# Kernel optimization log

Hardware: AMD Instinct MI355X
Metric: run time of the kernel (lower is better)

The kernel has to match this reference:

```python
import jax, jax.numpy as jnp
import numpy as np

KS = 5          # B-spline kernel_size per pseudo-coordinate dim
DIM = 2         # pseudo-coordinate dimensionality
NUM_GRAPHS = 64


def spline_conv(x, src, dst, edge_attr, W, root, bias):
    """Degree-1 open B-spline conv (torch-spline-conv semantics, aggr='mean').
    x: [N,Cin], edge_attr: [E,DIM] in [0,1], W: [KS**DIM,Cin,Cout]."""
    N = x.shape[0]
    E = src.shape[0]
    v = edge_attr * (KS - 1)                                   # [E,DIM]
    k_lo = jnp.clip(jnp.floor(v), 0, KS - 2).astype(jnp.int32) # lower knot index
    frac = v - k_lo.astype(v.dtype)                            # [E,DIM]
    # Precompute x @ W_k for all K kernel weights per node: [N,K,Cout]
    xW = jnp.einsum('nc,kco->nko', x, W)
    msg = jnp.zeros((E, W.shape[2]), x.dtype)
    # 2^DIM = 4 nonzero basis products for degree-1 splines
    for bits in ((0, 0), (0, 1), (1, 0), (1, 1)):
        b = jnp.ones((E,), x.dtype)
        wi = jnp.zeros((E,), jnp.int32)
        stride = 1
        for d, bit in enumerate(bits):
            b = b * (frac[:, d] if bit else (1.0 - frac[:, d]))
            wi = wi + (k_lo[:, d] + bit) * stride
            stride *= KS
        msg = msg + b[:, None] * xW[src, wi]                   # gather [E,Cout]
    agg = jax.ops.segment_sum(msg, dst, num_segments=N)
    deg = jax.ops.segment_sum(jnp.ones((E,), x.dtype), dst, num_segments=N)
    agg = agg / jnp.maximum(deg, 1.0)[:, None]                 # mean aggregation
    return agg + x @ root + bias


def setup_inputs() -> dict:
    key = jax.random.key(0)
    ks = jax.random.split(key, 12)
    N, E = 20000, 320000
    Cin, H, O = 1, 32, 10
    K = KS * KS
    p = lambda k, s: jax.random.normal(k, s, jnp.float32) * 0.1
    return {
        'x': jax.random.normal(ks[0], (N, Cin), jnp.float32),
        'edge_attr': jax.random.uniform(ks[1], (E, DIM), jnp.float32),
        'W1': p(ks[2], (K, Cin, H)), 'root1': p(ks[3], (Cin, H)), 'b1': jnp.zeros((H,), jnp.float32),
        'W2': p(ks[4], (K, H, 2 * H)), 'root2': p(ks[5], (H, 2 * H)), 'b2': jnp.zeros((2 * H,), jnp.float32),
        'Wf1': p(ks[6], (2 * H, 128)), 'bf1': jnp.zeros((128,), jnp.float32),
        'Wf2': p(ks[7], (128, O)), 'bf2': jnp.zeros((O,), jnp.float32),
        'edge_index': jax.random.randint(ks[8], (2, E), 0, N),
        'batch': jnp.sort(jax.random.randint(ks[9], (N,), 0, NUM_GRAPHS)),
    }


def reference(x, edge_attr, W1, root1, b1, W2, root2, b2, Wf1, bf1, Wf2, bf2, edge_index, batch):
    src, dst = edge_index[0], edge_index[1]
    h = jax.nn.relu(spline_conv(x, src, dst, edge_attr, W1, root1, b1))
    h = jax.nn.relu(spline_conv(h, src, dst, edge_attr, W2, root2, b2))
    # global mean pool over graphs
    gsum = jax.ops.segment_sum(h, batch, num_segments=NUM_GRAPHS)
    cnt = jax.ops.segment_sum(jnp.ones((h.shape[0],), h.dtype), batch, num_segments=NUM_GRAPHS)
    g = gsum / jnp.maximum(cnt, 1.0)[:, None]
    g = jax.nn.relu(g @ Wf1 + bf1)
    return jax.nn.log_softmax(g @ Wf2 + bf2, axis=1)
```

## Files before the change

### kernel.cpp

```cpp
#include <hip/hip_runtime.h>
#include <hip/hip_fp16.h>
#include <math.h>

#define KK 25
#define H1C 32
#define H2C 64
#define FCC 128
#define NCLS 10
#define NG 64
#define M1 32
#define M2 16

typedef _Float16 v8h __attribute__((ext_vector_type(8)));
typedef _Float16 v4h __attribute__((ext_vector_type(4)));
typedef float v4f __attribute__((ext_vector_type(4)));

__global__ __launch_bounds__(256) void deg_kernel(
    const int* __restrict__ edge_index, int E,
    int* __restrict__ degi,
    const float* __restrict__ W2, __half* __restrict__ W2t) {
    int i = blockIdx.x * 256 + threadIdx.x;
    if (i < KK * H2C * H1C) {
        int c = i & 31, o = (i >> 5) & 63, k = i >> 11;
        W2t[i] = __float2half(W2[(k * H1C + c) * H2C + o]);
    }
    if (i < E) atomicAdd(&degi[edge_index[E + i]], 1);
}

__global__ void scan1_kernel(const int* __restrict__ degi, int N,
                             int* __restrict__ incl, int* __restrict__ bsum) {
    __shared__ int s[256];
    int tid = threadIdx.x;
    int i = blockIdx.x * 256 + tid;
    int v = (i < N) ? degi[i] : 0;
    s[tid] = v;
    __syncthreads();
    for (int off = 1; off < 256; off <<= 1) {
        int t = (tid >= off) ? s[tid - off] : 0;
        __syncthreads();
        s[tid] += t;
        __syncthreads();
    }
    if (i < N) incl[i] = s[tid];
    if (tid == 255) bsum[blockIdx.x] = s[255];
}

__global__ void scan2_kernel(int* __restrict__ bsum, int nb) {
    __shared__ int s[256];
    int tid = threadIdx.x;
    int v = (tid < nb) ? bsum[tid] : 0;
    s[tid] = v;
    __syncthreads();
    for (int off = 1; off < 256; off <<= 1) {
        int t = (tid >= off) ? s[tid - off] : 0;
        __syncthreads();
        s[tid] += t;
        __syncthreads();
    }
    if (tid < nb) bsum[tid] = s[tid] - v;
}

__global__ void scan3_kernel(const int* __restrict__ incl, const int* __restrict__ degi,
                             const int* __restrict__ bsum, int N,
                             int* __restrict__ rowst, int* __restrict__ cur) {
    int i = blockIdx.x * 256 + threadIdx.x;
    if (i >= N) return;
    int r = incl[i] - degi[i] + bsum[blockIdx.x];
    rowst[i] = r;
    cur[i] = r;
}

__global__ void bucket_kernel(const float* __restrict__ edge_attr,
                              const int* __restrict__ edge_index, int E,
                              int* __restrict__ cur, int4* __restrict__ es) {
    int e = blockIdx.x * blockDim.x + threadIdx.x;
    if (e >= E) return;
    float v0 = edge_attr[2 * e + 0] * 4.0f;
    float v1 = edge_attr[2 * e + 1] * 4.0f;
    int k0 = (int)floorf(v0); k0 = min(max(k0, 0), 3);
    int k1 = (int)floorf(v1); k1 = min(max(k1, 0), 3);
    float f0 = v0 - (float)k0, f1 = v1 - (float)k1;
    int dst = edge_index[E + e];
    int pos = atomicAdd(&cur[dst], 1);
    es[pos] = make_int4(edge_index[e], (dst << 8) | (k0 + 5 * k1),
                        __float_as_int(f0), __float_as_int(f1));
}

__global__ __launch_bounds__(256) void l1_kernel(
    const float* __restrict__ x,
    const int* __restrict__ rowst, const int* __restrict__ degi,
    const int4* __restrict__ es,
    const float* __restrict__ W1, const float* __restrict__ root1,
    const float* __restrict__ b1, int N, int E,
    float* __restrict__ h1, __half* __restrict__ h1f) {
    __shared__ float w1s[KK * H1C];
    __shared__ float agg1[M1 * H1C];
    __shared__ int4 eb[8][32];
    __shared__ float xb[8][32];
    int tid = threadIdx.x;
    for (int i = tid; i < KK * H1C; i += 256) w1s[i] = W1[i];
    for (int i = tid; i < M1 * H1C; i += 256) agg1[i] = 0.0f;
    __syncthreads();
    int g = tid >> 5, o = tid & 31;
    int n0 = blockIdx.x * M1;
    int blkBeg = rowst[n0];
    int blkEnd = (n0 + M1 < N) ? rowst[n0 + M1] : E;
    int total = blkEnd - blkBeg;
    int per = (total + 7) >> 3;
    int wBeg = blkBeg + g * per;
    int wEnd = min(blkEnd, wBeg + per);
    int curDst = -1;
    float acc = 0.0f;
    for (int base = wBeg; base < wEnd; base += 32) {
        int m = min(32, wEnd - base);
        if (o < m) {
            int4 ed = es[base + o];
            eb[g][o] = ed;
            xb[g][o] = x[ed.x];
        }
        for (int j = 0; j < m; j++) {
            int4 ed = eb[g][j];
            float xs = xb[g][j];
            int dst = ed.y >> 8;
            if (dst != curDst) {
                if (curDst >= 0) atomicAdd(&agg1[(curDst - n0) * H1C + o], acc);
                acc = 0.0f;
                curDst = dst;
            }
            float f0 = __int_as_float(ed.z), f1 = __int_as_float(ed.w);
            float g0 = 1.0f - f0, g1 = 1.0f - f1;
            int kb = (ed.y & 0xff) << 5;
            float coef = g0 * g1 * w1s[kb + o] + f0 * g1 * w1s[kb + 32 + o] +
                         g0 * f1 * w1s[kb + 160 + o] + f0 * f1 * w1s[kb + 192 + o];
            acc = fmaf(xs, coef, acc);
        }
    }
    if (curDst >= 0) atomicAdd(&agg1[(curDst - n0) * H1C + o], acc);
    __syncthreads();
#pragma unroll
    for (int i = 0; i < 4; i++) {
        int ln = g + 8 * i;
        int n = n0 + ln;
        if (n < N) {
            float rdeg = 1.0f / fmaxf((float)degi[n], 1.0f);
            float hv = fmaxf(agg1[ln * H1C + o] * rdeg + x[n] * root1[o] + b1[o], 0.0f);
            h1[n * H1C + o] = hv;
            h1f[n * H1C + o] = __float2half(hv);
        }
    }
}

__global__ __launch_bounds__(256) void xw2m_kernel(
    const __half* __restrict__ h1f,
    const __half* __restrict__ W2t,
    int N, __half* __restrict__ xph) {
    int wv = threadIdx.x >> 6;
    int lane = threadIdx.x & 63;
    int r15 = lane & 15, quad = lane >> 4;
    int n0 = blockIdx.x * 16;
    int o0 = wv * 16;
    v8h bfrag = {};
    int bn = n0 + r15;
    bool wr = bn < N;
    if (wr) bfrag = *(const v8h*)(h1f + (size_t)bn * H1C + quad * 8);
    size_t baseoff = (size_t)bn * (KK * H2C) + o0 + (quad << 2);
    for (int k = 0; k < KK; k++) {
        v8h afrag = *(const v8h*)(W2t + ((k << 6) + o0 + r15) * H1C + quad * 8);
        v4f acc = {};
        acc = __builtin_amdgcn_mfma_f32_16x16x32_f16(afrag, bfrag, acc, 0, 0, 0);
        if (wr) {
            v4h hv;
            hv[0] = (_Float16)acc[0];
            hv[1] = (_Float16)acc[1];
            hv[2] = (_Float16)acc[2];
            hv[3] = (_Float16)acc[3];
            *(v4h*)(xph + baseoff + (k << 6)) = hv;
        }
    }
}

__global__ __launch_bounds__(256) void l2_kernel(
    const float* __restrict__ h1,
    const int* __restrict__ rowst, const int* __restrict__ degi,
    const int4* __restrict__ es,
    const unsigned* __restrict__ xphu,
    const float* __restrict__ root2, const float* __restrict__ b2,
    const int* __restrict__ batch,
    int N, int E, float* __restrict__ gsum) {
    __shared__ float agg[M2 * H2C];
    __shared__ int4 eb[4][64];
    int tid = threadIdx.x;
    for (int i = tid; i < M2 * H2C; i += 256) agg[i] = 0.0f;
    __syncthreads();
    int w = tid >> 6, lane = tid & 63;
    int o2 = lane & 31, eh = lane >> 5;
    int n0 = blockIdx.x * M2;
    int blkBeg = rowst[n0];
    int blkEnd = (n0 + M2 < N) ? rowst[n0 + M2] : E;
    int total = blkEnd - blkBeg;
    int per = (total + 3) >> 2;
    int wBeg = blkBeg + w * per;
    int wEnd = min(blkEnd, wBeg + per);
    int curDst = -1;
    float ax = 0.0f, ay = 0.0f;
    for (int base = wBeg; base < wEnd; base += 64) {
        int m = min(64, wEnd - base);
        if (lane < m) eb[w][lane] = es[base + lane];
        for (int j = 0; j < m; j += 2) {
            int jj = j + eh;
            bool act = jj < m;
            int4 ed = eb[w][act ? jj : j];
            const unsigned* p = xphu + (size_t)ed.x * (KK * H2C / 2) +
                                ((ed.y & 0xff) << 5) + o2;
            unsigned t0 = p[0], t1 = p[32], t2 = p[160], t3 = p[192];
            if (act) {
                int dst = ed.y >> 8;
                if (dst != curDst) {
                    if (curDst >= 0) {
                        atomicAdd(&agg[(curDst - n0) * H2C + 2 * o2], ax);
                        atomicAdd(&agg[(curDst - n0) * H2C + 2 * o2 + 1], ay);
                    }
                    ax = ay = 0.0f;
                    curDst = dst;
                }
                float f0 = __int_as_float(ed.z), f1 = __int_as_float(ed.w);
                float g0 = 1.0f - f0, g1 = 1.0f - f1;
                float b0 = g0 * g1, b1 = f0 * g1, bb2 = g0 * f1, b3 = f0 * f1;
                __half2 h0 = *(__half2*)&t0, h1v = *(__half2*)&t1;
                __half2 h2 = *(__half2*)&t2, h3 = *(__half2*)&t3;
                ax = fmaf(b0, __low2float(h0), ax);  ay = fmaf(b0, __high2float(h0), ay);
                ax = fmaf(b1, __low2float(h1v), ax); ay = fmaf(b1, __high2float(h1v), ay);
                ax = fmaf(bb2, __low2float(h2), ax); ay = fmaf(bb2, __high2float(h2), ay);
                ax = fmaf(b3, __low2float(h3), ax);  ay = fmaf(b3, __high2float(h3), ay);
            }
        }
    }
    if (curDst >= 0) {
        atomicAdd(&agg[(curDst - n0) * H2C + 2 * o2], ax);
        atomicAdd(&agg[(curDst - n0) * H2C + 2 * o2 + 1], ay);
    }
    __syncthreads();

#pragma unroll
    for (int i = 0; i < 4; i++) {
        int ln = w + 4 * i;
        int n = n0 + ln;
        if (n < N) {
            float rd = 1.0f / fmaxf((float)degi[n], 1.0f);
            float v = agg[ln * H2C + lane] * rd + b2[lane];
            const float* hr = h1 + n * H1C;
#pragma unroll 8
            for (int c = 0; c < H1C; c++) v = fmaf(hr[c], root2[c * H2C + lane], v);
            agg[ln * H2C + lane] = fmaxf(v, 0.0f);
        } else {
            agg[ln * H2C + lane] = 0.0f;
        }
    }
    __syncthreads();

    if (tid < H2C) {
        float run = 0.0f;
        int curg = batch[n0];
        for (int ln = 0; ln < M2; ln++) {
            int n = n0 + ln;
            if (n >= N) break;
            int gg = batch[n];
            if (gg != curg) {
                atomicAdd(&gsum[curg * H2C + tid], run);
                run = 0.0f;
                curg = gg;
            }
            run += agg[ln * H2C + tid];
        }
        atomicAdd(&gsum[curg * H2C + tid], run);
    }
}

__global__ void head_kernel(const float* __restrict__ gsum,
                            const int* __restrict__ batch, int N,
                            const float* __restrict__ Wf1, const float* __restrict__ bf1,
                            const float* __restrict__ Wf2, const float* __restrict__ bf2,
                            float* __restrict__ out) {
    __shared__ float gc[H2C];
    __shared__ float t1[FCC];
    __shared__ float lg[NCLS];
    __shared__ float lse;
    __shared__ float scnt;
    int g = blockIdx.x, tid = threadIdx.x;
    if (tid == 0) {
        int lo = 0, hi = N;
        while (lo < hi) { int m = (lo + hi) >> 1; if (batch[m] < g) lo = m + 1; else hi = m; }
        int lb = lo;
        lo = 0; hi = N;
        while (lo < hi) { int m = (lo + hi) >> 1; if (batch[m] <= g) lo = m + 1; else hi = m; }
        scnt = (float)(lo - lb);
    }
    __syncthreads();
    if (tid < H2C) gc[tid] = gsum[g * H2C + tid] / fmaxf(scnt, 1.0f);
    __syncthreads();
    {
        float acc = bf1[tid];
        for (int c = 0; c < H2C; c++) acc += gc[c] * Wf1[c * FCC + tid];
        t1[tid] = fmaxf(acc, 0.0f);
    }
    __syncthreads();
    if (tid < NCLS) {
        float acc = bf2[tid];
        for (int j = 0; j < FCC; j++) acc += t1[j] * Wf2[j * NCLS + tid];
        lg[tid] = acc;
    }
    __syncthreads();
    if (tid == 0) {
        float m = lg[0];
        for (int c = 1; c < NCLS; c++) m = fmaxf(m, lg[c]);
        float s = 0.0f;
        for (int c = 0; c < NCLS; c++) s += expf(lg[c] - m);
        lse = m + logf(s);
    }
    __syncthreads();
    if (tid < NCLS) out[g * NCLS + tid] = lg[tid] - lse;
}

extern "C" void kernel_launch(void* const* d_in, const int* in_sizes, int n_in,
                              void* d_out, int out_size, void* d_ws, size_t ws_size,
                              hipStream_t stream) {
    const float* x          = (const float*)d_in[0];
    const float* edge_attr  = (const float*)d_in[1];
    const float* W1         = (const float*)d_in[2];
    const float* root1      = (const float*)d_in[3];
    const float* b1         = (const float*)d_in[4];
    const float* W2         = (const float*)d_in[5];
    const float* root2      = (const float*)d_in[6];
    const float* b2         = (const float*)d_in[7];
    const float* Wf1        = (const float*)d_in[8];
    const float* bf1        = (const float*)d_in[9];
    const float* Wf2        = (const float*)d_in[10];
    const float* bf2        = (const float*)d_in[11];
    const int*   edge_index = (const int*)d_in[12];
    const int*   batch      = (const int*)d_in[13];
    float* out = (float*)d_out;

    const int N = in_sizes[13];
    const int E = in_sizes[12] / 2;
    const int NB = (N + 255) / 256;

    int4*     es   = (int4*)d_ws;
    unsigned* xphu = (unsigned*)(es + E);
    __half*   w2t  = (__half*)(xphu + (size_t)N * 800);
    __half*   h1f  = w2t + KK * H2C * H1C;
    float* gsum  = (float*)(h1f + (size_t)N * H1C);
    int*   degi  = (int*)(gsum + NG * H2C);
    int*   rowst = degi + N;
    int*   cur   = rowst + N;
    int*   incl  = cur + N;
    int*   bsum  = incl + N;
    float* h1    = (float*)(bsum + 256);

    hipMemsetAsync(gsum, 0, (size_t)NG * H2C * sizeof(float) + (size_t)N * sizeof(int),
                   stream);

    const int W2TN = KK * H2C * H1C;
    int degBlocks = (max(E, W2TN) + 255) / 256;
    deg_kernel<<<degBlocks, 256, 0, stream>>>(edge_index, E, degi, W2, w2t);

    scan1_kernel<<<NB, 256, 0, stream>>>(degi, N, incl, bsum);
    scan2_kernel<<<1, 256, 0, stream>>>(bsum, NB);
    scan3_kernel<<<NB, 256, 0, stream>>>(incl, degi, bsum, N, rowst, cur);

    bucket_kernel<<<(E + 255) / 256, 256, 0, stream>>>(edge_attr, edge_index, E, cur, es);

    l1_kernel<<<(N + M1 - 1) / M1, 256, 0, stream>>>(
        x, rowst, degi, es, W1, root1, b1, N, E, h1, h1f);

    xw2m_kernel<<<(N + 15) / 16, 256, 0, stream>>>(h1f, w2t, N, (__half*)xphu);

    l2_kernel<<<(N + M2 - 1) / M2, 256, 0, stream>>>(
        h1, rowst, degi, es, xphu, root2, b2, batch, N, E, gsum);

    head_kernel<<<NG, FCC, 0, stream>>>(gsum, batch, N, Wf1, bf1, Wf2, bf2, out);
}
```

Measured before the change: 215.4 us.

## Aggregate basis-weighted inputs before the W2 matmul and fuse the layer-2 kernels

Reorders layer 2 from transform-then-aggregate to aggregate-then-transform. Each block scatters basis-weighted h1 features into a per-node shared-memory buffer of size K*Cin using LDS atomics. It then applies W2 and root2 with MFMA inside the same kernel. This removes the large per-node xW intermediate (N*25*64 halfs) and its global write/read traffic, along with the fp32 h1 copy. In exchange it adds four LDS float atomics per edge-channel, uses about 51KB of shared memory per block, which may limit occupancy, and rounds the aggregated sums to fp16 before the MFMA.

Result: slower. 425.8 us (+97.6%).

```diff
diff --git a/kernel.cpp b/kernel.cpp
--- a/kernel.cpp
+++ b/kernel.cpp
@@ -10,19 +10,24 @@
 #define NG 64
 #define M1 32
 #define M2 16
+#define SROW 804
 
 typedef _Float16 v8h __attribute__((ext_vector_type(8)));
-typedef _Float16 v4h __attribute__((ext_vector_type(4)));
 typedef float v4f __attribute__((ext_vector_type(4)));
 
 __global__ __launch_bounds__(256) void deg_kernel(
     const int* __restrict__ edge_index, int E,
     int* __restrict__ degi,
-    const float* __restrict__ W2, __half* __restrict__ W2t) {
+    const float* __restrict__ W2, __half* __restrict__ W2o,
+    const float* __restrict__ root2, __half* __restrict__ r2t) {
     int i = blockIdx.x * 256 + threadIdx.x;
-    if (i < KK * H2C * H1C) {
-        int c = i & 31, o = (i >> 5) & 63, k = i >> 11;
-        W2t[i] = __float2half(W2[(k * H1C + c) * H2C + o]);
+    if (i < KK * H1C * H2C) {
+        int o = i & 63, kc = i >> 6;
+        W2o[(size_t)o * (KK * H1C) + kc] = __float2half(W2[i]);
+    }
+    if (i < H1C * H2C) {
+        int o = i & 63, c = i >> 6;
+        r2t[o * H1C + c] = __float2half(root2[i]);
     }
     if (i < E) atomicAdd(&degi[edge_index[E + i]], 1);
 }
@@ -92,7 +97,7 @@
     const int4* __restrict__ es,
     const float* __restrict__ W1, const float* __restrict__ root1,
     const float* __restrict__ b1, int N, int E,
-    float* __restrict__ h1, __half* __restrict__ h1f) {
+    __half* __restrict__ h1f) {
     __shared__ float w1s[KK * H1C];
     __shared__ float agg1[M1 * H1C];
     __shared__ int4 eb[8][32];
@@ -144,54 +149,27 @@
         if (n < N) {
             float rdeg = 1.0f / fmaxf((float)degi[n], 1.0f);
             float hv = fmaxf(agg1[ln * H1C + o] * rdeg + x[n] * root1[o] + b1[o], 0.0f);
-            h1[n * H1C + o] = hv;
             h1f[n * H1C + o] = __float2half(hv);
         }
     }
 }
 
-__global__ __launch_bounds__(256) void xw2m_kernel(
+__global__ __launch_bounds__(256) void l2f_kernel(
     const __half* __restrict__ h1f,
-    const __half* __restrict__ W2t,
-    int N, __half* __restrict__ xph) {
-    int wv = threadIdx.x >> 6;
-    int lane = threadIdx.x & 63;
-    int r15 = lane & 15, quad = lane >> 4;
-    int n0 = blockIdx.x * 16;
-    int o0 = wv * 16;
-    v8h bfrag = {};
-    int bn = n0 + r15;
-    bool wr = bn < N;
-    if (wr) bfrag = *(const v8h*)(h1f + (size_t)bn * H1C + quad * 8);
-    size_t baseoff = (size_t)bn * (KK * H2C) + o0 + (quad << 2);
-    for (int k = 0; k < KK; k++) {
-        v8h afrag = *(const v8h*)(W2t + ((k << 6) + o0 + r15) * H1C + quad * 8);
-        v4f acc = {};
-        acc = __builtin_amdgcn_mfma_f32_16x16x32_f16(afrag, bfrag, acc, 0, 0, 0);
-        if (wr) {
-            v4h hv;
-            hv[0] = (_Float16)acc[0];
-            hv[1] = (_Float16)acc[1];
-            hv[2] = (_Float16)acc[2];
-            hv[3] = (_Float16)acc[3];
-            *(v4h*)(xph + baseoff + (k << 6)) = hv;
-        }
-    }
-}
-
-__global__ __launch_bounds__(256) void l2_kernel(
-    const float* __restrict__ h1,
     const int* __restrict__ rowst, const int* __restrict__ degi,
     const int4* __restrict__ es,
-    const unsigned* __restrict__ xphu,
-    const float* __restrict__ root2, const float* __restrict__ b2,
+    const __half* __restrict__ W2o,
+    const __half* __restrict__ r2t,
+    const float* __restrict__ b2,
     const int* __restrict__ batch,
     int N, int E, float* __restrict__ gsum) {
-    __shared__ float agg[M2 * H2C];
+    __shared__ float S[M2 * SROW];
     __shared__ int4 eb[4][64];
+    __shared__ float h2s[M2 * H2C];
     int tid = threadIdx.x;
-    for (int i = tid; i < M2 * H2C; i += 256) agg[i] = 0.0f;
-    __syncthreads();
+    for (int i = tid; i < M2 * SROW; i += 256) S[i] = 0.0f;
+    __syncthreads();
+
     int w = tid >> 6, lane = tid & 63;
     int o2 = lane & 31, eh = lane >> 5;
     int n0 = blockIdx.x * M2;
@@ -201,60 +179,66 @@
     int per = (total + 3) >> 2;
     int wBeg = blkBeg + w * per;
     int wEnd = min(blkEnd, wBeg + per);
-    int curDst = -1;
-    float ax = 0.0f, ay = 0.0f;
+
     for (int base = wBeg; base < wEnd; base += 64) {
         int m = min(64, wEnd - base);
         if (lane < m) eb[w][lane] = es[base + lane];
         for (int j = 0; j < m; j += 2) {
             int jj = j + eh;
-            bool act = jj < m;
-            int4 ed = eb[w][act ? jj : j];
-            const unsigned* p = xphu + (size_t)ed.x * (KK * H2C / 2) +
-                                ((ed.y & 0xff) << 5) + o2;
-            unsigned t0 = p[0], t1 = p[32], t2 = p[160], t3 = p[192];
-            if (act) {
-                int dst = ed.y >> 8;
-                if (dst != curDst) {
-                    if (curDst >= 0) {
-                        atomicAdd(&agg[(curDst - n0) * H2C + 2 * o2], ax);
-                        atomicAdd(&agg[(curDst - n0) * H2C + 2 * o2 + 1], ay);
-                    }
-                    ax = ay = 0.0f;
-                    curDst = dst;
-                }
+            if (jj < m) {
+                int4 ed = eb[w][jj];
+                float xv = __half2float(h1f[(size_t)ed.x * H1C + o2]);
+                int dstl = (ed.y >> 8) - n0;
+                int kb = ed.y & 0xff;
                 float f0 = __int_as_float(ed.z), f1 = __int_as_float(ed.w);
                 float g0 = 1.0f - f0, g1 = 1.0f - f1;
-                float b0 = g0 * g1, b1 = f0 * g1, bb2 = g0 * f1, b3 = f0 * f1;
-                __half2 h0 = *(__half2*)&t0, h1v = *(__half2*)&t1;
-                __half2 h2 = *(__half2*)&t2, h3 = *(__half2*)&t3;
-                ax = fmaf(b0, __low2float(h0), ax);  ay = fmaf(b0, __high2float(h0), ay);
-                ax = fmaf(b1, __low2float(h1v), ax); ay = fmaf(b1, __high2float(h1v), ay);
-                ax = fmaf(bb2, __low2float(h2), ax); ay = fmaf(bb2, __high2float(h2), ay);
-                ax = fmaf(b3, __low2float(h3), ax);  ay = fmaf(b3, __high2float(h3), ay);
+                float* row = &S[dstl * SROW + (kb << 5) + o2];
+                atomicAdd(row,       g0 * g1 * xv);
+                atomicAdd(row + 32,  f0 * g1 * xv);
+                atomicAdd(row + 160, g0 * f1 * xv);
+                atomicAdd(row + 192, f0 * f1 * xv);
             }
         }
     }
-    if (curDst >= 0) {
-        atomicAdd(&agg[(curDst - n0) * H2C + 2 * o2], ax);
-        atomicAdd(&agg[(curDst - n0) * H2C + 2 * o2 + 1], ay);
-    }
-    __syncthreads();
-
+    __syncthreads();
+
+    int r15 = lane & 15, quad = lane >> 4;
+    int o0 = w * 16;
+    v4f acc = {};
+    v4f acc2 = {};
+    const float* arow = &S[r15 * SROW + quad * 8];
+    const __half* brow = W2o + (size_t)(o0 + r15) * (KK * H1C) + quad * 8;
 #pragma unroll
-    for (int i = 0; i < 4; i++) {
-        int ln = w + 4 * i;
+    for (int kk = 0; kk < KK; kk++) {
+        v4f lo = *(const v4f*)(arow + (kk << 5));
+        v4f hi = *(const v4f*)(arow + (kk << 5) + 4);
+        v8h ah;
+        ah[0] = (_Float16)lo[0]; ah[1] = (_Float16)lo[1];
+        ah[2] = (_Float16)lo[2]; ah[3] = (_Float16)lo[3];
+        ah[4] = (_Float16)hi[0]; ah[5] = (_Float16)hi[1];
+        ah[6] = (_Float16)hi[2]; ah[7] = (_Float16)hi[3];
+        v8h bh = *(const v8h*)(brow + (kk << 5));
+        acc = __builtin_amdgcn_mfma_f32_16x16x32_f16(ah, bh, acc, 0, 0, 0);
+    }
+    {
+        int an = n0 + r15;
+        v8h ah = {};
+        if (an < N) ah = *(const v8h*)(h1f + (size_t)an * H1C + quad * 8);
+        v8h bh = *(const v8h*)(r2t + (o0 + r15) * H1C + quad * 8);
+        acc2 = __builtin_amdgcn_mfma_f32_16x16x32_f16(ah, bh, acc2, 0, 0, 0);
+    }
+    int oo = o0 + r15;
+    float bb = b2[oo];
+#pragma unroll
+    for (int r = 0; r < 4; r++) {
+        int ln = quad * 4 + r;
         int n = n0 + ln;
+        float v = 0.0f;
         if (n < N) {
             float rd = 1.0f / fmaxf((float)degi[n], 1.0f);
-            float v = agg[ln * H2C + lane] * rd + b2[lane];
-            const float* hr = h1 + n * H1C;
-#pragma unroll 8
-            for (int c = 0; c < H1C; c++) v = fmaf(hr[c], root2[c * H2C + lane], v);
-            agg[ln * H2C + lane] = fmaxf(v, 0.0f);
-        } else {
-            agg[ln * H2C + lane] = 0.0f;
-        }
+            v = fmaxf(acc[r] * rd + acc2[r] + bb, 0.0f);
+        }
+        h2s[ln * H2C + oo] = v;
     }
     __syncthreads();
 
@@ -270,7 +254,7 @@
                 run = 0.0f;
                 curg = gg;
             }
-            run += agg[ln * H2C + tid];
+            run += h2s[ln * H2C + tid];
         }
         atomicAdd(&gsum[curg * H2C + tid], run);
     }
@@ -344,24 +328,22 @@
     const int E = in_sizes[12] / 2;
     const int NB = (N + 255) / 256;
 
-    int4*     es   = (int4*)d_ws;
-    unsigned* xphu = (unsigned*)(es + E);
-    __half*   w2t  = (__half*)(xphu + (size_t)N * 800);
-    __half*   h1f  = w2t + KK * H2C * H1C;
-    float* gsum  = (float*)(h1f + (size_t)N * H1C);
-    int*   degi  = (int*)(gsum + NG * H2C);
+    int4*   es  = (int4*)d_ws;
+    __half* W2o = (__half*)(es + E);
+    __half* r2t = W2o + (size_t)H2C * KK * H1C;
+    __half* h1f = r2t + H2C * H1C;
+    float* gsum = (float*)(h1f + (size_t)N * H1C);
+    int*   degi = (int*)(gsum + NG * H2C);
     int*   rowst = degi + N;
     int*   cur   = rowst + N;
     int*   incl  = cur + N;
     int*   bsum  = incl + N;
-    float* h1    = (float*)(bsum + 256);
 
     hipMemsetAsync(gsum, 0, (size_t)NG * H2C * sizeof(float) + (size_t)N * sizeof(int),
                    stream);
 
-    const int W2TN = KK * H2C * H1C;
-    int degBlocks = (max(E, W2TN) + 255) / 256;
-    deg_kernel<<<degBlocks, 256, 0, stream>>>(edge_index, E, degi, W2, w2t);
+    int degBlocks = (E + 255) / 256;
+    deg_kernel<<<degBlocks, 256, 0, stream>>>(edge_index, E, degi, W2, W2o, root2, r2t);
 
     scan1_kernel<<<NB, 256, 0, stream>>>(degi, N, incl, bsum);
     scan2_kernel<<<1, 256, 0, stream>>>(bsum, NB);
@@ -370,12 +352,10 @@
     bucket_kernel<<<(E + 255) / 256, 256, 0, stream>>>(edge_attr, edge_index, E, cur, es);
 
     l1_kernel<<<(N + M1 - 1) / M1, 256, 0, stream>>>(
-        x, rowst, degi, es, W1, root1, b1, N, E, h1, h1f);
-
-    xw2m_kernel<<<(N + 15) / 16, 256, 0, stream>>>(h1f, w2t, N, (__half*)xphu);
-
-    l2_kernel<<<(N + M2 - 1) / M2, 256, 0, stream>>>(
-        h1, rowst, degi, es, xphu, root2, b2, batch, N, E, gsum);
+        x, rowst, degi, es, W1, root1, b1, N, E, h1f);
+
+    l2f_kernel<<<(N + M2 - 1) / M2, 256, 0, stream>>>(
+        h1f, rowst, degi, es, W2o, r2t, b2, batch, N, E, gsum);
 
     head_kernel<<<NG, FCC, 0, stream>>>(gsum, batch, N, Wf1, bf1, Wf2, bf2, out);
 }
```
